# Performance work log

Measured on AMD Instinct MI355X. Metric: run time of the kernel, lower is better.

Reference implementation:

```python
import jax, jax.numpy as jnp
import numpy as np
import math

INPUT_DIM = 1024
EMBED_DIM = 1024
NUM_HEADS = 16
HEAD_DIM = EMBED_DIM // NUM_HEADS


def setup_inputs() -> dict:
    key = jax.random.key(0)
    k_x, k_qkv, k_out_w, k_out_b = jax.random.split(key, 4)
    x = jax.random.normal(k_x, (1, 4096, INPUT_DIM), dtype=jnp.float32)
    # nn.Linear weights are [out, in]; kaiming-uniform-ish scale
    s1 = 1.0 / math.sqrt(INPUT_DIM)
    s2 = 1.0 / math.sqrt(EMBED_DIM)
    qkv_w = jax.random.uniform(k_qkv, (3 * EMBED_DIM, INPUT_DIM), jnp.float32, -s1, s1)
    out_w = jax.random.uniform(k_out_w, (EMBED_DIM, EMBED_DIM), jnp.float32, -s2, s2)
    out_b = jax.random.uniform(k_out_b, (EMBED_DIM,), jnp.float32, -s2, s2)
    return {"x": x, "qkv_w": qkv_w, "out_w": out_w, "out_b": out_b}


def reference(x, qkv_w, out_w, out_b):
    B, N, C = x.shape
    qkv = jnp.einsum('bnc,ec->bne', x, qkv_w)  # [B,N,3E]
    q = qkv[:, :, 0:EMBED_DIM].reshape(B, N, NUM_HEADS, HEAD_DIM)
    k = qkv[:, :, EMBED_DIM:2 * EMBED_DIM].reshape(B, N, NUM_HEADS, HEAD_DIM)
    v = qkv[:, :, 2 * EMBED_DIM:].reshape(B, N, NUM_HEADS, HEAD_DIM)
    scores = jnp.einsum('bihd,bjhd->bhij', q, k) / jnp.sqrt(jnp.float32(HEAD_DIM))
    attn = jax.nn.softmax(scores, axis=-1)  # [B,H,N,N]
    out = jnp.einsum('bhik,bkhd->bhid', attn, v)
    out = out.transpose(0, 2, 1, 3).reshape(B, N, EMBED_DIM)
    return jnp.einsum('bne,fe->bnf', out, out_w) + out_b
```

## Files before the change

kernel.cpp:

```cpp
#include <hip/hip_runtime.h>
#include <hip/hip_bf16.h>

typedef __bf16 bf16;
typedef bf16 bf16x8 __attribute__((ext_vector_type(8)));
typedef bf16 bf16x4 __attribute__((ext_vector_type(4)));
typedef float f32x4 __attribute__((ext_vector_type(4)));

#define MFMA16(a, b, c) __builtin_amdgcn_mfma_f32_16x16x32_bf16(a, b, c, 0, 0, 0)

__device__ __forceinline__ void g2l16(const bf16* g, bf16* l) {
  __builtin_amdgcn_global_load_lds(
      (__attribute__((address_space(1))) void*)(void*)g,
      (__attribute__((address_space(3))) void*)l,
      16, 0, 0);
}

__global__ void sniff_dtype(const void* __restrict__ x, int* __restrict__ flag) {
  const unsigned short* u = (const unsigned short*)x;
  const int lane = threadIdx.x;
  unsigned short v = u[lane];
  int e = (v >> 7) & 0xFF;
  int sane = (e == 0) || (e >= 112 && e <= 142);
  unsigned long long m = __ballot(sane);
  if (lane == 0) flag[0] = (__popcll(m) >= 56) ? 1 : 0;
}

__global__ void convert_to_bf16(const void* __restrict__ in, bf16* __restrict__ out,
                                long n8, const int* __restrict__ flag) {
  long i = (long)blockIdx.x * 256 + threadIdx.x;
  if (i >= n8) return;
  if (*flag) {
    ((bf16x8*)out)[i] = ((const bf16x8*)in)[i];
  } else {
    const float4* p = (const float4*)in;
    float4 a = p[i * 2], b = p[i * 2 + 1];
    bf16x8 v;
    v[0] = (bf16)a.x; v[1] = (bf16)a.y; v[2] = (bf16)a.z; v[3] = (bf16)a.w;
    v[4] = (bf16)b.x; v[5] = (bf16)b.y; v[6] = (bf16)b.z; v[7] = (bf16)b.w;
    ((bf16x8*)out)[i] = v;
  }
}

__global__ __launch_bounds__(256) void gemm_qkv(
    const bf16* __restrict__ A, const bf16* __restrict__ B,
    bf16* __restrict__ qB, bf16* __restrict__ kP, bf16* __restrict__ vP) {
  __shared__ __align__(16) bf16 As[128 * 32];
  __shared__ __align__(16) bf16 Bs[128 * 32];

  const int tid  = threadIdx.x;
  const int lane = tid & 63;
  const int wave = tid >> 6;
  const int wm   = wave >> 1, wn = wave & 1;
  const int l15  = lane & 15, quad = lane >> 4;
  const long m0 = (long)blockIdx.x * 128;
  const long n0 = (long)blockIdx.y * 128;
  const int  K  = 1024;

  const bf16* Ab = A + m0 * K;
  const bf16* Bb = B + n0 * K;
  const int rowA = tid & 127;
  const int dc   = tid >> 7;

  f32x4 acc[4][4] = {};

  for (int k0 = 0; k0 < K; k0 += 32) {
    g2l16(Ab + (long)rowA * K + k0 + dc * 8,       As + tid * 8);
    g2l16(Ab + (long)rowA * K + k0 + (dc + 2) * 8, As + (tid + 256) * 8);
    g2l16(Bb + (long)rowA * K + k0 + dc * 8,       Bs + tid * 8);
    g2l16(Bb + (long)rowA * K + k0 + (dc + 2) * 8, Bs + (tid + 256) * 8);
    __syncthreads();

    bf16x8 af[4], bfr[4];
#pragma unroll
    for (int t = 0; t < 4; t++) {
      af[t]  = *(const bf16x8*)(As + (quad * 128 + wm * 64 + t * 16 + l15) * 8);
      bfr[t] = *(const bf16x8*)(Bs + (quad * 128 + wn * 64 + t * 16 + l15) * 8);
    }
#pragma unroll
    for (int tm = 0; tm < 4; tm++)
#pragma unroll
      for (int tn = 0; tn < 4; tn++)
        acc[tm][tn] = MFMA16(af[tm], bfr[tn], acc[tm][tn]);
    __syncthreads();
  }

  const long rb = m0 + wm * 64;
  const long cb = n0 + wn * 64;
  const int third = (int)(n0 >> 10);
  const float QSC = 0.125f * 1.44269504088896f;

#pragma unroll
  for (int tm = 0; tm < 4; tm++) {
#pragma unroll
    for (int tn = 0; tn < 4; tn++) {
      const long r0 = rb + tm * 16 + quad * 4;
      const long c  = cb + tn * 16 + l15;
      if (third == 0) {
#pragma unroll
        for (int r = 0; r < 4; r++)
          qB[(r0 + r) * 1024 + c] = (bf16)(acc[tm][tn][r] * QSC);
      } else if (third == 1) {
        const int ep = (int)c - 1024;
        const int h = ep >> 6, d = ep & 63;
        const long bhd = (long)h * 64 * 4096 + (long)((d >> 3) * 64) * 8 + (d & 7);
#pragma unroll
        for (int r = 0; r < 4; r++) {
          const int n = (int)(r0 + r);
          const int kt = n >> 6, kpos = n & 63;
          const int tn_ = 2 * (kpos >> 5) + ((kpos >> 2) & 1);
          const int m   = tn_ * 16 + ((kpos >> 3) & 3) * 4 + (kpos & 3);
          kP[bhd + (long)kt * 4096 + m * 8] = (bf16)acc[tm][tn][r];
        }
      } else {
        const int ep = (int)c - 2048;
        const int h = ep >> 6, d = ep & 63;
        const int n0r = (int)r0;
        const int kt = n0r >> 6, pc = (n0r & 63) >> 3;
        bf16x4 v;
#pragma unroll
        for (int r = 0; r < 4; r++) v[r] = (bf16)acc[tm][tn][r];
        *(bf16x4*)(vP + (long)(h * 64 + kt) * 4096 + (pc * 64 + d) * 8 +
                   (quad & 1) * 4) = v;
      }
    }
  }
}

template <bool BIAS, bool DYNOUT>
__global__ __launch_bounds__(256) void gemm_bt(
    const bf16* __restrict__ A, const bf16* __restrict__ B,
    void* __restrict__ Cv, const bf16* __restrict__ bias,
    int M, int Nn, int K, const int* __restrict__ oflag) {
  __shared__ __align__(16) bf16 As[128 * 32];
  __shared__ __align__(16) bf16 Bs[128 * 32];

  const int tid  = threadIdx.x;
  const int lane = tid & 63;
  const int wave = tid >> 6;
  const int wm   = wave >> 1, wn = wave & 1;
  const int l15  = lane & 15, quad = lane >> 4;
  const long m0 = (long)blockIdx.x * 128;
  const long n0 = (long)blockIdx.y * 128;

  const bf16* Ab = A + m0 * K;
  const bf16* Bb = B + n0 * K;
  const int rowA = tid & 127;
  const int dc   = tid >> 7;

  f32x4 acc[4][4] = {};

  for (int k0 = 0; k0 < K; k0 += 32) {
    g2l16(Ab + (long)rowA * K + k0 + dc * 8,       As + tid * 8);
    g2l16(Ab + (long)rowA * K + k0 + (dc + 2) * 8, As + (tid + 256) * 8);
    g2l16(Bb + (long)rowA * K + k0 + dc * 8,       Bs + tid * 8);
    g2l16(Bb + (long)rowA * K + k0 + (dc + 2) * 8, Bs + (tid + 256) * 8);
    __syncthreads();

    bf16x8 af[4], bfr[4];
#pragma unroll
    for (int t = 0; t < 4; t++) {
      af[t]  = *(const bf16x8*)(As + (quad * 128 + wm * 64 + t * 16 + l15) * 8);
      bfr[t] = *(const bf16x8*)(Bs + (quad * 128 + wn * 64 + t * 16 + l15) * 8);
    }
#pragma unroll
    for (int tm = 0; tm < 4; tm++)
#pragma unroll
      for (int tn = 0; tn < 4; tn++)
        acc[tm][tn] = MFMA16(af[tm], bfr[tn], acc[tm][tn]);
    __syncthreads();
  }

  const int obf = DYNOUT ? *oflag : 1;
  const long rb = m0 + wm * 64;
  const long cb = n0 + wn * 64;
#pragma unroll
  for (int tm = 0; tm < 4; tm++) {
#pragma unroll
    for (int tn = 0; tn < 4; tn++) {
      const long r0 = rb + tm * 16 + quad * 4;
      const long c  = cb + tn * 16 + l15;
      const float bv = BIAS ? (float)bias[c] : 0.0f;
#pragma unroll
      for (int r = 0; r < 4; r++) {
        const float val = acc[tm][tn][r] + bv;
        const long idx = (r0 + r) * Nn + c;
        if (DYNOUT && !obf) ((float*)Cv)[idx] = val;
        else                ((bf16*)Cv)[idx]  = (bf16)val;
      }
    }
  }
}

__global__ __launch_bounds__(256) void flash_attn(
    const bf16* __restrict__ qB, const bf16* __restrict__ kP,
    const bf16* __restrict__ vP, bf16* __restrict__ O) {
  __shared__ __align__(16) bf16 Ks[2][64 * 64];
  __shared__ __align__(16) bf16 Vs[2][64 * 64];

  const int tid = threadIdx.x;
  const int lane = tid & 63;
  const int wave = tid >> 6;
  const int l15 = lane & 15, quad = lane >> 4;
  const int bid = blockIdx.x;
  const int xcd = bid & 7, bi = bid >> 3;
  const int h  = xcd + 8 * (bi >> 5);
  const int qt = bi & 31;
  const int q0 = qt * 128;

  bf16x8 qf[2][2];
#pragma unroll
  for (int g = 0; g < 2; g++) {
    const bf16* qrow = qB + (long)(q0 + wave * 32 + g * 16 + l15) * 1024 + h * 64;
    qf[g][0] = *(const bf16x8*)(qrow + quad * 8);
    qf[g][1] = *(const bf16x8*)(qrow + 32 + quad * 8);
  }

  bf16x8 onesf;
#pragma unroll
  for (int j = 0; j < 8; j++) onesf[j] = (bf16)1.0f;

  f32x4 oa[2][4] = {};
  f32x4 la[2] = {};

  const bf16* kb = kP + (long)h * 64 * 4096;
  const bf16* vb = vP + (long)h * 64 * 4096;

#pragma unroll
  for (int i = 0; i < 2; i++) {
    g2l16(kb + (tid + i * 256) * 8, Ks[0] + (tid + i * 256) * 8);
    g2l16(vb + (tid + i * 256) * 8, Vs[0] + (tid + i * 256) * 8);
  }

  for (int kt = 0; kt < 64; kt++) {
    const int cur = kt & 1;
    __syncthreads();
    if (kt + 1 < 64) {
      const bf16* kbase = kb + (long)(kt + 1) * 4096;
      const bf16* vbase = vb + (long)(kt + 1) * 4096;
#pragma unroll
      for (int i = 0; i < 2; i++) {
        g2l16(kbase + (tid + i * 256) * 8, Ks[cur ^ 1] + (tid + i * 256) * 8);
        g2l16(vbase + (tid + i * 256) * 8, Vs[cur ^ 1] + (tid + i * 256) * 8);
      }
    }

    f32x4 s[2][4];
#pragma unroll
    for (int tn = 0; tn < 4; tn++) {
      bf16x8 a0 = *(const bf16x8*)(Ks[cur] + ((quad)*64 + tn * 16 + l15) * 8);
      bf16x8 a1 = *(const bf16x8*)(Ks[cur] + ((4 + quad) * 64 + tn * 16 + l15) * 8);
      f32x4 z0 = {}; z0 = MFMA16(a0, qf[0][0], z0); z0 = MFMA16(a1, qf[0][1], z0);
      f32x4 z1 = {}; z1 = MFMA16(a0, qf[1][0], z1); z1 = MFMA16(a1, qf[1][1], z1);
      s[0][tn] = z0; s[1][tn] = z1;
    }

    bf16x8 pf[2][2];
#pragma unroll
    for (int g = 0; g < 2; g++)
#pragma unroll
      for (int tn = 0; tn < 4; tn++)
#pragma unroll
        for (int r = 0; r < 4; r++)
          pf[g][tn >> 1][(tn & 1) * 4 + r] =
              (bf16)__builtin_amdgcn_exp2f(s[g][tn][r]);

#pragma unroll
    for (int tm = 0; tm < 4; tm++) {
      bf16x8 v0 = *(const bf16x8*)(Vs[cur] + ((quad)*64 + tm * 16 + l15) * 8);
      bf16x8 v1 = *(const bf16x8*)(Vs[cur] + ((4 + quad) * 64 + tm * 16 + l15) * 8);
      oa[0][tm] = MFMA16(v0, pf[0][0], oa[0][tm]);
      oa[0][tm] = MFMA16(v1, pf[0][1], oa[0][tm]);
      oa[1][tm] = MFMA16(v0, pf[1][0], oa[1][tm]);
      oa[1][tm] = MFMA16(v1, pf[1][1], oa[1][tm]);
    }
#pragma unroll
    for (int g = 0; g < 2; g++) {
      la[g] = MFMA16(onesf, pf[g][0], la[g]);
      la[g] = MFMA16(onesf, pf[g][1], la[g]);
    }
  }

#pragma unroll
  for (int g = 0; g < 2; g++) {
    const float inv = 1.0f / la[g][0];
    bf16* orow = O + (long)(q0 + wave * 32 + g * 16 + l15) * 1024 + h * 64;
#pragma unroll
    for (int tm = 0; tm < 4; tm++) {
      bf16x4 v;
#pragma unroll
      for (int r = 0; r < 4; r++) v[r] = (bf16)(oa[g][tm][r] * inv);
      *(bf16x4*)(orow + tm * 16 + quad * 4) = v;
    }
  }
}

extern "C" void kernel_launch(void* const* d_in, const int* in_sizes, int n_in,
                              void* d_out, int out_size, void* d_ws, size_t ws_size,
                              hipStream_t stream) {
  const void* x     = d_in[0];
  const void* qkv_w = d_in[1];
  const void* out_w = d_in[2];
  const void* out_b = d_in[3];

  char* ws = (char*)d_ws;
  int*  flag = (int*)ws;
  bf16* qB   = (bf16*)(ws + 4096);
  bf16* kP   = (bf16*)(ws + 4096 + 8388608);
  bf16* vP   = (bf16*)(ws + 4096 + 16777216);
  bf16* ob   = (bf16*)(ws + 4096 + 25165824);
  bf16* qwb  = (bf16*)(ws + 4096 + 33554432);
  bf16* xb   = ob;
  bf16* owb  = qB;
  bf16* obb  = qB + 1048576;

  sniff_dtype<<<1, 64, 0, stream>>>(x, flag);
  convert_to_bf16<<<2048, 256, 0, stream>>>(x, xb, 524288, flag);
  convert_to_bf16<<<1536, 256, 0, stream>>>(qkv_w, qwb, 393216, flag);

  gemm_qkv<<<dim3(32, 24), 256, 0, stream>>>(xb, qwb, qB, kP, vP);

  flash_attn<<<512, 256, 0, stream>>>(qB, kP, vP, ob);

  convert_to_bf16<<<512, 256, 0, stream>>>(out_w, owb, 131072, flag);
  convert_to_bf16<<<1, 256, 0, stream>>>(out_b, obb, 128, flag);

  gemm_bt<true, true><<<dim3(32, 8), 256, 0, stream>>>(
      ob, owb, d_out, obb, 4096, 1024, 1024, flag);
}
```

Before: 269.7 us.

## Split KV sequence across waves in flash attention with per-wave buffers

Each block now handles 64 queries and each wave processes a quarter of the key/value sequence with its own double-buffered LDS region. This removes block-wide barriers inside the main loop and replaces them with per-wave waitcnt. Partial outputs and row sums are reduced across waves through LDS at the end. The QKV GEMM epilogue writes K and V in a new 32-row tile layout to match, and the grid doubles to 1024 blocks. The cost is an extra LDS reduction and more LDS per block.

```diff
diff --git a/kernel.cpp b/kernel.cpp
--- a/kernel.cpp
+++ b/kernel.cpp
@@ -102,25 +102,24 @@
       } else if (third == 1) {
         const int ep = (int)c - 1024;
         const int h = ep >> 6, d = ep & 63;
-        const long bhd = (long)h * 64 * 4096 + (long)((d >> 3) * 64) * 8 + (d & 7);
 #pragma unroll
         for (int r = 0; r < 4; r++) {
           const int n = (int)(r0 + r);
-          const int kt = n >> 6, kpos = n & 63;
-          const int tn_ = 2 * (kpos >> 5) + ((kpos >> 2) & 1);
-          const int m   = tn_ * 16 + ((kpos >> 3) & 3) * 4 + (kpos & 3);
-          kP[bhd + (long)kt * 4096 + m * 8] = (bf16)acc[tm][tn][r];
+          const int si = n >> 5, k = n & 31;
+          const int sig = ((k >> 2) & 1) * 16 + (k >> 3) * 4 + (k & 3);
+          kP[((long)h * 128 + si) * 2048 +
+             ((d >> 3) * 32 + sig) * 8 + (d & 7)] = (bf16)acc[tm][tn][r];
         }
       } else {
         const int ep = (int)c - 2048;
         const int h = ep >> 6, d = ep & 63;
         const int n0r = (int)r0;
-        const int kt = n0r >> 6, pc = (n0r & 63) >> 3;
+        const int si = n0r >> 5, k0 = n0r & 31;
         bf16x4 v;
 #pragma unroll
         for (int r = 0; r < 4; r++) v[r] = (bf16)acc[tm][tn][r];
-        *(bf16x4*)(vP + (long)(h * 64 + kt) * 4096 + (pc * 64 + d) * 8 +
-                   (quad & 1) * 4) = v;
+        *(bf16x4*)(vP + ((long)h * 128 + si) * 2048 +
+                   ((k0 >> 3) * 64 + d) * 8 + (quad & 1) * 4) = v;
       }
     }
   }
@@ -194,8 +193,8 @@
 __global__ __launch_bounds__(256) void flash_attn(
     const bf16* __restrict__ qB, const bf16* __restrict__ kP,
     const bf16* __restrict__ vP, bf16* __restrict__ O) {
-  __shared__ __align__(16) bf16 Ks[2][64 * 64];
-  __shared__ __align__(16) bf16 Vs[2][64 * 64];
+  __shared__ __align__(16) bf16 Sbuf[4][2][4096];
+  __shared__ float lred[4][4][16];
 
   const int tid = threadIdx.x;
   const int lane = tid & 63;
@@ -203,14 +202,14 @@
   const int l15 = lane & 15, quad = lane >> 4;
   const int bid = blockIdx.x;
   const int xcd = bid & 7, bi = bid >> 3;
-  const int h  = xcd + 8 * (bi >> 5);
-  const int qt = bi & 31;
-  const int q0 = qt * 128;
-
-  bf16x8 qf[2][2];
-#pragma unroll
-  for (int g = 0; g < 2; g++) {
-    const bf16* qrow = qB + (long)(q0 + wave * 32 + g * 16 + l15) * 1024 + h * 64;
+  const int h  = xcd + 8 * (bi >> 6);
+  const int qt = bi & 63;
+  const int q0 = qt * 64;
+
+  bf16x8 qf[4][2];
+#pragma unroll
+  for (int g = 0; g < 4; g++) {
+    const bf16* qrow = qB + (long)(q0 + g * 16 + l15) * 1024 + h * 64;
     qf[g][0] = *(const bf16x8*)(qrow + quad * 8);
     qf[g][1] = *(const bf16x8*)(qrow + 32 + quad * 8);
   }
@@ -219,78 +218,90 @@
 #pragma unroll
   for (int j = 0; j < 8; j++) onesf[j] = (bf16)1.0f;
 
-  f32x4 oa[2][4] = {};
-  f32x4 la[2] = {};
-
-  const bf16* kb = kP + (long)h * 64 * 4096;
-  const bf16* vb = vP + (long)h * 64 * 4096;
-
-#pragma unroll
-  for (int i = 0; i < 2; i++) {
-    g2l16(kb + (tid + i * 256) * 8, Ks[0] + (tid + i * 256) * 8);
-    g2l16(vb + (tid + i * 256) * 8, Vs[0] + (tid + i * 256) * 8);
-  }
-
-  for (int kt = 0; kt < 64; kt++) {
-    const int cur = kt & 1;
-    __syncthreads();
-    if (kt + 1 < 64) {
-      const bf16* kbase = kb + (long)(kt + 1) * 4096;
-      const bf16* vbase = vb + (long)(kt + 1) * 4096;
-#pragma unroll
-      for (int i = 0; i < 2; i++) {
-        g2l16(kbase + (tid + i * 256) * 8, Ks[cur ^ 1] + (tid + i * 256) * 8);
-        g2l16(vbase + (tid + i * 256) * 8, Vs[cur ^ 1] + (tid + i * 256) * 8);
+  f32x4 oa[4][4] = {};
+  f32x4 la[4] = {};
+
+  const bf16* kb = kP + ((long)h * 128 + wave * 32) * 2048;
+  const bf16* vb = vP + ((long)h * 128 + wave * 32) * 2048;
+  bf16* buf0 = Sbuf[wave][0];
+  bf16* buf1 = Sbuf[wave][1];
+
+#pragma unroll
+  for (int i = 0; i < 4; i++) {
+    g2l16(kb + (lane + i * 64) * 8, buf0 + (lane + i * 64) * 8);
+    g2l16(vb + (lane + i * 64) * 8, buf0 + 2048 + (lane + i * 64) * 8);
+  }
+
+  for (int t = 0; t < 32; t++) {
+    const int cur = t & 1;
+    const long nt = (long)((t + 1) & 31) * 2048;
+    bf16* nb = cur ? buf0 : buf1;
+#pragma unroll
+    for (int i = 0; i < 4; i++) {
+      g2l16(kb + nt + (lane + i * 64) * 8, nb + (lane + i * 64) * 8);
+      g2l16(vb + nt + (lane + i * 64) * 8, nb + 2048 + (lane + i * 64) * 8);
+    }
+    __builtin_amdgcn_s_waitcnt(0x0F78);
+
+    const bf16* kg = cur ? buf1 : buf0;
+    const bf16* vg = kg + 2048;
+
+    bf16x8 pf[4];
+#pragma unroll
+    for (int kh = 0; kh < 2; kh++) {
+      bf16x8 a0 = *(const bf16x8*)(kg + ((quad)*32 + kh * 16 + l15) * 8);
+      bf16x8 a1 = *(const bf16x8*)(kg + ((4 + quad) * 32 + kh * 16 + l15) * 8);
+      f32x4 z[4];
+#pragma unroll
+      for (int g = 0; g < 4; g++) {
+        f32x4 zz = {};
+        zz = MFMA16(a0, qf[g][0], zz);
+        zz = MFMA16(a1, qf[g][1], zz);
+        z[g] = zz;
       }
-    }
-
-    f32x4 s[2][4];
-#pragma unroll
-    for (int tn = 0; tn < 4; tn++) {
-      bf16x8 a0 = *(const bf16x8*)(Ks[cur] + ((quad)*64 + tn * 16 + l15) * 8);
-      bf16x8 a1 = *(const bf16x8*)(Ks[cur] + ((4 + quad) * 64 + tn * 16 + l15) * 8);
-      f32x4 z0 = {}; z0 = MFMA16(a0, qf[0][0], z0); z0 = MFMA16(a1, qf[0][1], z0);
-      f32x4 z1 = {}; z1 = MFMA16(a0, qf[1][0], z1); z1 = MFMA16(a1, qf[1][1], z1);
-      s[0][tn] = z0; s[1][tn] = z1;
-    }
-
-    bf16x8 pf[2][2];
-#pragma unroll
-    for (int g = 0; g < 2; g++)
-#pragma unroll
-      for (int tn = 0; tn < 4; tn++)
+#pragma unroll
+      for (int g = 0; g < 4; g++)
 #pragma unroll
         for (int r = 0; r < 4; r++)
-          pf[g][tn >> 1][(tn & 1) * 4 + r] =
-              (bf16)__builtin_amdgcn_exp2f(s[g][tn][r]);
-
-#pragma unroll
-    for (int tm = 0; tm < 4; tm++) {
-      bf16x8 v0 = *(const bf16x8*)(Vs[cur] + ((quad)*64 + tm * 16 + l15) * 8);
-      bf16x8 v1 = *(const bf16x8*)(Vs[cur] + ((4 + quad) * 64 + tm * 16 + l15) * 8);
-      oa[0][tm] = MFMA16(v0, pf[0][0], oa[0][tm]);
-      oa[0][tm] = MFMA16(v1, pf[0][1], oa[0][tm]);
-      oa[1][tm] = MFMA16(v0, pf[1][0], oa[1][tm]);
-      oa[1][tm] = MFMA16(v1, pf[1][1], oa[1][tm]);
-    }
-#pragma unroll
-    for (int g = 0; g < 2; g++) {
-      la[g] = MFMA16(onesf, pf[g][0], la[g]);
-      la[g] = MFMA16(onesf, pf[g][1], la[g]);
-    }
-  }
-
-#pragma unroll
-  for (int g = 0; g < 2; g++) {
-    const float inv = 1.0f / la[g][0];
-    bf16* orow = O + (long)(q0 + wave * 32 + g * 16 + l15) * 1024 + h * 64;
-#pragma unroll
-    for (int tm = 0; tm < 4; tm++) {
-      bf16x4 v;
-#pragma unroll
-      for (int r = 0; r < 4; r++) v[r] = (bf16)(oa[g][tm][r] * inv);
-      *(bf16x4*)(orow + tm * 16 + quad * 4) = v;
-    }
+          pf[g][kh * 4 + r] = (bf16)__builtin_amdgcn_exp2f(z[g][r]);
+    }
+
+#pragma unroll
+    for (int dt = 0; dt < 4; dt++) {
+      bf16x8 v = *(const bf16x8*)(vg + (quad * 64 + dt * 16 + l15) * 8);
+#pragma unroll
+      for (int g = 0; g < 4; g++) oa[dt][g] = MFMA16(v, pf[g], oa[dt][g]);
+    }
+#pragma unroll
+    for (int g = 0; g < 4; g++) la[g] = MFMA16(onesf, pf[g], la[g]);
+  }
+
+  float* lds_f = (float*)Sbuf;
+  float* mine = lds_f + wave * 4096;
+#pragma unroll
+  for (int dt = 0; dt < 4; dt++)
+#pragma unroll
+    for (int g = 0; g < 4; g++)
+      *(f32x4*)(mine + (dt * 4 + g) * 256 + lane * 4) = oa[dt][g];
+  if (quad == 0)
+#pragma unroll
+    for (int g = 0; g < 4; g++) lred[wave][g][l15] = la[g][0];
+  __syncthreads();
+
+#pragma unroll
+  for (int g = 0; g < 4; g++) {
+    f32x4 acc = {};
+#pragma unroll
+    for (int u = 0; u < 4; u++)
+      acc += *(const f32x4*)(lds_f + u * 4096 + (wave * 4 + g) * 256 + lane * 4);
+    const float l = lred[0][g][l15] + lred[1][g][l15] +
+                    lred[2][g][l15] + lred[3][g][l15];
+    const float inv = 1.0f / l;
+    bf16x4 v;
+#pragma unroll
+    for (int r = 0; r < 4; r++) v[r] = (bf16)(acc[r] * inv);
+    *(bf16x4*)(O + (long)(q0 + g * 16 + l15) * 1024 + h * 64 + wave * 16 +
+               quad * 4) = v;
   }
 }
 
@@ -319,7 +330,7 @@
 
   gemm_qkv<<<dim3(32, 24), 256, 0, stream>>>(xb, qwb, qB, kP, vP);
 
-  flash_attn<<<512, 256, 0, stream>>>(qB, kP, vP, ob);
+  flash_attn<<<1024, 256, 0, stream>>>(qB, kP, vP, ob);
 
   convert_to_bf16<<<512, 256, 0, stream>>>(out_w, owb, 131072, flag);
   convert_to_bf16<<<1, 256, 0, stream>>>(out_b, obb, 128, flag);
```

New measurement: 270.6 us. No clear change (+0.3%).

## Halve flash-attention query tile to double grid and merge convert launches

Applied to the files above, without the earlier changes.

Flash attention now processes 64 query rows per block (16 per wave) instead of 128, doubling the grid to 1024 blocks and cutting per-wave accumulator registers. This aims to improve occupancy and latency hiding, at the cost of doubled K/V loads and a higher LDS-read-to-MFMA ratio. Separately, pairs of dtype-conversion launches are fused into a single kernel to reduce launch overhead.

```diff
diff --git a/kernel.cpp b/kernel.cpp
--- a/kernel.cpp
+++ b/kernel.cpp
@@ -25,11 +25,8 @@
   if (lane == 0) flag[0] = (__popcll(m) >= 56) ? 1 : 0;
 }
 
-__global__ void convert_to_bf16(const void* __restrict__ in, bf16* __restrict__ out,
-                                long n8, const int* __restrict__ flag) {
-  long i = (long)blockIdx.x * 256 + threadIdx.x;
-  if (i >= n8) return;
-  if (*flag) {
+__device__ __forceinline__ void conv8(const void* in, bf16* out, long i, int f) {
+  if (f) {
     ((bf16x8*)out)[i] = ((const bf16x8*)in)[i];
   } else {
     const float4* p = (const float4*)in;
@@ -39,6 +36,16 @@
     v[4] = (bf16)b.x; v[5] = (bf16)b.y; v[6] = (bf16)b.z; v[7] = (bf16)b.w;
     ((bf16x8*)out)[i] = v;
   }
+}
+
+__global__ void convert2_to_bf16(const void* __restrict__ a, bf16* __restrict__ oa,
+                                 long na8, const void* __restrict__ b,
+                                 bf16* __restrict__ ob, long nb8,
+                                 const int* __restrict__ flag) {
+  long i = (long)blockIdx.x * 256 + threadIdx.x;
+  const int f = *flag;
+  if (i < na8) conv8(a, oa, i, f);
+  else if (i - na8 < nb8) conv8(b, ob, i - na8, f);
 }
 
 __global__ __launch_bounds__(256) void gemm_qkv(
@@ -194,8 +201,8 @@
 __global__ __launch_bounds__(256) void flash_attn(
     const bf16* __restrict__ qB, const bf16* __restrict__ kP,
     const bf16* __restrict__ vP, bf16* __restrict__ O) {
-  __shared__ __align__(16) bf16 Ks[2][64 * 64];
-  __shared__ __align__(16) bf16 Vs[2][64 * 64];
+  __shared__ __align__(16) bf16 Ks[2][4096];
+  __shared__ __align__(16) bf16 Vs[2][4096];
 
   const int tid = threadIdx.x;
   const int lane = tid & 63;
@@ -203,24 +210,23 @@
   const int l15 = lane & 15, quad = lane >> 4;
   const int bid = blockIdx.x;
   const int xcd = bid & 7, bi = bid >> 3;
-  const int h  = xcd + 8 * (bi >> 5);
-  const int qt = bi & 31;
-  const int q0 = qt * 128;
-
-  bf16x8 qf[2][2];
-#pragma unroll
-  for (int g = 0; g < 2; g++) {
-    const bf16* qrow = qB + (long)(q0 + wave * 32 + g * 16 + l15) * 1024 + h * 64;
-    qf[g][0] = *(const bf16x8*)(qrow + quad * 8);
-    qf[g][1] = *(const bf16x8*)(qrow + 32 + quad * 8);
+  const int h  = xcd + 8 * (bi >> 6);
+  const int qt = bi & 63;
+  const int q0 = qt * 64;
+
+  bf16x8 qf[2];
+  {
+    const bf16* qrow = qB + (long)(q0 + wave * 16 + l15) * 1024 + h * 64;
+    qf[0] = *(const bf16x8*)(qrow + quad * 8);
+    qf[1] = *(const bf16x8*)(qrow + 32 + quad * 8);
   }
 
   bf16x8 onesf;
 #pragma unroll
   for (int j = 0; j < 8; j++) onesf[j] = (bf16)1.0f;
 
-  f32x4 oa[2][4] = {};
-  f32x4 la[2] = {};
+  f32x4 oa[4] = {};
+  f32x4 la = {};
 
   const bf16* kb = kP + (long)h * 64 * 4096;
   const bf16* vb = vP + (long)h * 64 * 4096;
@@ -244,53 +250,44 @@
       }
     }
 
-    f32x4 s[2][4];
+    f32x4 s[4];
 #pragma unroll
     for (int tn = 0; tn < 4; tn++) {
       bf16x8 a0 = *(const bf16x8*)(Ks[cur] + ((quad)*64 + tn * 16 + l15) * 8);
       bf16x8 a1 = *(const bf16x8*)(Ks[cur] + ((4 + quad) * 64 + tn * 16 + l15) * 8);
-      f32x4 z0 = {}; z0 = MFMA16(a0, qf[0][0], z0); z0 = MFMA16(a1, qf[0][1], z0);
-      f32x4 z1 = {}; z1 = MFMA16(a0, qf[1][0], z1); z1 = MFMA16(a1, qf[1][1], z1);
-      s[0][tn] = z0; s[1][tn] = z1;
-    }
-
-    bf16x8 pf[2][2];
-#pragma unroll
-    for (int g = 0; g < 2; g++)
-#pragma unroll
-      for (int tn = 0; tn < 4; tn++)
-#pragma unroll
-        for (int r = 0; r < 4; r++)
-          pf[g][tn >> 1][(tn & 1) * 4 + r] =
-              (bf16)__builtin_amdgcn_exp2f(s[g][tn][r]);
+      f32x4 z = {};
+      z = MFMA16(a0, qf[0], z);
+      z = MFMA16(a1, qf[1], z);
+      s[tn] = z;
+    }
+
+    bf16x8 pf[2];
+#pragma unroll
+    for (int tn = 0; tn < 4; tn++)
+#pragma unroll
+      for (int r = 0; r < 4; r++)
+        pf[tn >> 1][(tn & 1) * 4 + r] =
+            (bf16)__builtin_amdgcn_exp2f(s[tn][r]);
 
 #pragma unroll
     for (int tm = 0; tm < 4; tm++) {
       bf16x8 v0 = *(const bf16x8*)(Vs[cur] + ((quad)*64 + tm * 16 + l15) * 8);
       bf16x8 v1 = *(const bf16x8*)(Vs[cur] + ((4 + quad) * 64 + tm * 16 + l15) * 8);
-      oa[0][tm] = MFMA16(v0, pf[0][0], oa[0][tm]);
-      oa[0][tm] = MFMA16(v1, pf[0][1], oa[0][tm]);
-      oa[1][tm] = MFMA16(v0, pf[1][0], oa[1][tm]);
-      oa[1][tm] = MFMA16(v1, pf[1][1], oa[1][tm]);
-    }
-#pragma unroll
-    for (int g = 0; g < 2; g++) {
-      la[g] = MFMA16(onesf, pf[g][0], la[g]);
-      la[g] = MFMA16(onesf, pf[g][1], la[g]);
-    }
-  }
-
-#pragma unroll
-  for (int g = 0; g < 2; g++) {
-    const float inv = 1.0f / la[g][0];
-    bf16* orow = O + (long)(q0 + wave * 32 + g * 16 + l15) * 1024 + h * 64;
-#pragma unroll
-    for (int tm = 0; tm < 4; tm++) {
-      bf16x4 v;
-#pragma unroll
-      for (int r = 0; r < 4; r++) v[r] = (bf16)(oa[g][tm][r] * inv);
-      *(bf16x4*)(orow + tm * 16 + quad * 4) = v;
-    }
+      oa[tm] = MFMA16(v0, pf[0], oa[tm]);
+      oa[tm] = MFMA16(v1, pf[1], oa[tm]);
+    }
+    la = MFMA16(onesf, pf[0], la);
+    la = MFMA16(onesf, pf[1], la);
+  }
+
+  const float inv = 1.0f / la[0];
+  bf16* orow = O + (long)(q0 + wave * 16 + l15) * 1024 + h * 64;
+#pragma unroll
+  for (int tm = 0; tm < 4; tm++) {
+    bf16x4 v;
+#pragma unroll
+    for (int r = 0; r < 4; r++) v[r] = (bf16)(oa[tm][r] * inv);
+    *(bf16x4*)(orow + tm * 16 + quad * 4) = v;
   }
 }
 
@@ -314,15 +311,13 @@
   bf16* obb  = qB + 1048576;
 
   sniff_dtype<<<1, 64, 0, stream>>>(x, flag);
-  convert_to_bf16<<<2048, 256, 0, stream>>>(x, xb, 524288, flag);
-  convert_to_bf16<<<1536, 256, 0, stream>>>(qkv_w, qwb, 393216, flag);
+  convert2_to_bf16<<<3584, 256, 0, stream>>>(x, xb, 524288, qkv_w, qwb, 393216, flag);
 
   gemm_qkv<<<dim3(32, 24), 256, 0, stream>>>(xb, qwb, qB, kP, vP);
 
-  flash_attn<<<512, 256, 0, stream>>>(qB, kP, vP, ob);
-
-  convert_to_bf16<<<512, 256, 0, stream>>>(out_w, owb, 131072, flag);
-  convert_to_bf16<<<1, 256, 0, stream>>>(out_b, obb, 128, flag);
+  flash_attn<<<1024, 256, 0, stream>>>(qB, kP, vP, ob);
+
+  convert2_to_bf16<<<513, 256, 0, stream>>>(out_w, owb, 131072, out_b, obb, 128, flag);
 
   gemm_bt<true, true><<<dim3(32, 8), 256, 0, stream>>>(
       ob, owb, d_out, obb, 4096, 1024, 1024, flag);
```

After: 261.2 us. -3.2%, faster.

## Restructure flash attention to 2-wave blocks with V in registers and merged converts

Applied to the files above, without the earlier changes.

The attention kernel now uses 128-thread blocks with 64 query rows each, doubling the grid. Only K is staged into LDS, while V tiles are loaded straight from global memory into registers and double-buffered across an unrolled two-step loop. The row-sum is accumulated in scalar registers and reduced with shuffles, replacing the extra ones-matrix MFMAs. Pairs of dtype-conversion launches are merged into single kernels to cut launch count. The trade-offs are higher register pressure from the V buffers and K/V being loaded twice as often in total because of the smaller query tile.

```diff
diff --git a/kernel.cpp b/kernel.cpp
--- a/kernel.cpp
+++ b/kernel.cpp
@@ -25,11 +25,8 @@
   if (lane == 0) flag[0] = (__popcll(m) >= 56) ? 1 : 0;
 }
 
-__global__ void convert_to_bf16(const void* __restrict__ in, bf16* __restrict__ out,
-                                long n8, const int* __restrict__ flag) {
-  long i = (long)blockIdx.x * 256 + threadIdx.x;
-  if (i >= n8) return;
-  if (*flag) {
+__device__ __forceinline__ void conv8(const void* in, bf16* out, long i, int f) {
+  if (f) {
     ((bf16x8*)out)[i] = ((const bf16x8*)in)[i];
   } else {
     const float4* p = (const float4*)in;
@@ -39,6 +36,16 @@
     v[4] = (bf16)b.x; v[5] = (bf16)b.y; v[6] = (bf16)b.z; v[7] = (bf16)b.w;
     ((bf16x8*)out)[i] = v;
   }
+}
+
+__global__ void convert2_to_bf16(const void* __restrict__ a, bf16* __restrict__ oa,
+                                 long na8, const void* __restrict__ b,
+                                 bf16* __restrict__ ob, long nb8,
+                                 const int* __restrict__ flag) {
+  long i = (long)blockIdx.x * 256 + threadIdx.x;
+  const int f = *flag;
+  if (i < na8) conv8(a, oa, i, f);
+  else if (i - na8 < nb8) conv8(b, ob, i - na8, f);
 }
 
 __global__ __launch_bounds__(256) void gemm_qkv(
@@ -191,11 +198,10 @@
   }
 }
 
-__global__ __launch_bounds__(256) void flash_attn(
+__global__ __launch_bounds__(128, 2) void flash_attn(
     const bf16* __restrict__ qB, const bf16* __restrict__ kP,
     const bf16* __restrict__ vP, bf16* __restrict__ O) {
-  __shared__ __align__(16) bf16 Ks[2][64 * 64];
-  __shared__ __align__(16) bf16 Vs[2][64 * 64];
+  __shared__ __align__(16) bf16 Ks[2][4096];
 
   const int tid = threadIdx.x;
   const int lane = tid & 63;
@@ -203,9 +209,9 @@
   const int l15 = lane & 15, quad = lane >> 4;
   const int bid = blockIdx.x;
   const int xcd = bid & 7, bi = bid >> 3;
-  const int h  = xcd + 8 * (bi >> 5);
-  const int qt = bi & 31;
-  const int q0 = qt * 128;
+  const int h  = xcd + 8 * (bi >> 6);
+  const int qt = bi & 63;
+  const int q0 = qt * 64;
 
   bf16x8 qf[2][2];
 #pragma unroll
@@ -215,74 +221,88 @@
     qf[g][1] = *(const bf16x8*)(qrow + 32 + quad * 8);
   }
 
-  bf16x8 onesf;
-#pragma unroll
-  for (int j = 0; j < 8; j++) onesf[j] = (bf16)1.0f;
-
   f32x4 oa[2][4] = {};
-  f32x4 la[2] = {};
+  float l_sum[2] = {0.0f, 0.0f};
 
   const bf16* kb = kP + (long)h * 64 * 4096;
   const bf16* vb = vP + (long)h * 64 * 4096;
 
-#pragma unroll
-  for (int i = 0; i < 2; i++) {
-    g2l16(kb + (tid + i * 256) * 8, Ks[0] + (tid + i * 256) * 8);
-    g2l16(vb + (tid + i * 256) * 8, Vs[0] + (tid + i * 256) * 8);
-  }
-
-  for (int kt = 0; kt < 64; kt++) {
-    const int cur = kt & 1;
-    __syncthreads();
-    if (kt + 1 < 64) {
-      const bf16* kbase = kb + (long)(kt + 1) * 4096;
-      const bf16* vbase = vb + (long)(kt + 1) * 4096;
-#pragma unroll
-      for (int i = 0; i < 2; i++) {
-        g2l16(kbase + (tid + i * 256) * 8, Ks[cur ^ 1] + (tid + i * 256) * 8);
-        g2l16(vbase + (tid + i * 256) * 8, Vs[cur ^ 1] + (tid + i * 256) * 8);
-      }
-    }
-
+  const int voff_lo = (quad * 64 + l15) * 8;
+  const int voff_hi = ((4 + quad) * 64 + l15) * 8;
+
+  auto stageK = [&](int t, bf16* dst) {
+    const bf16* src = kb + (long)t * 4096;
+#pragma unroll
+    for (int i = 0; i < 4; i++)
+      g2l16(src + (tid + i * 128) * 8, dst + (tid + i * 128) * 8);
+  };
+  auto loadV = [&](int t, bf16x8* vr) {
+    const bf16* vt = vb + (long)t * 4096;
+#pragma unroll
+    for (int tm = 0; tm < 4; tm++) {
+      vr[tm]     = *(const bf16x8*)(vt + voff_lo + tm * 128);
+      vr[4 + tm] = *(const bf16x8*)(vt + voff_hi + tm * 128);
+    }
+  };
+  auto compute = [&](const bf16* kbuf, const bf16x8* vr) {
     f32x4 s[2][4];
 #pragma unroll
     for (int tn = 0; tn < 4; tn++) {
-      bf16x8 a0 = *(const bf16x8*)(Ks[cur] + ((quad)*64 + tn * 16 + l15) * 8);
-      bf16x8 a1 = *(const bf16x8*)(Ks[cur] + ((4 + quad) * 64 + tn * 16 + l15) * 8);
+      bf16x8 a0 = *(const bf16x8*)(kbuf + ((quad)*64 + tn * 16 + l15) * 8);
+      bf16x8 a1 = *(const bf16x8*)(kbuf + ((4 + quad) * 64 + tn * 16 + l15) * 8);
       f32x4 z0 = {}; z0 = MFMA16(a0, qf[0][0], z0); z0 = MFMA16(a1, qf[0][1], z0);
       f32x4 z1 = {}; z1 = MFMA16(a0, qf[1][0], z1); z1 = MFMA16(a1, qf[1][1], z1);
       s[0][tn] = z0; s[1][tn] = z1;
     }
-
     bf16x8 pf[2][2];
 #pragma unroll
-    for (int g = 0; g < 2; g++)
-#pragma unroll
-      for (int tn = 0; tn < 4; tn++)
-#pragma unroll
-        for (int r = 0; r < 4; r++)
-          pf[g][tn >> 1][(tn & 1) * 4 + r] =
-              (bf16)__builtin_amdgcn_exp2f(s[g][tn][r]);
-
+    for (int g = 0; g < 2; g++) {
+#pragma unroll
+      for (int hh = 0; hh < 2; hh++) {
+        union { bf16x8 v; __hip_bfloat162 h2[4]; } u;
+#pragma unroll
+        for (int j = 0; j < 4; j++) {
+          const int tn = hh * 2 + (j >> 1);
+          const int r  = (j & 1) * 2;
+          float p0 = __builtin_amdgcn_exp2f(s[g][tn][r]);
+          float p1 = __builtin_amdgcn_exp2f(s[g][tn][r + 1]);
+          l_sum[g] += p0 + p1;
+          u.h2[j] = __float22bfloat162_rn(float2{p0, p1});
+        }
+        pf[g][hh] = u.v;
+      }
+    }
 #pragma unroll
     for (int tm = 0; tm < 4; tm++) {
-      bf16x8 v0 = *(const bf16x8*)(Vs[cur] + ((quad)*64 + tm * 16 + l15) * 8);
-      bf16x8 v1 = *(const bf16x8*)(Vs[cur] + ((4 + quad) * 64 + tm * 16 + l15) * 8);
-      oa[0][tm] = MFMA16(v0, pf[0][0], oa[0][tm]);
-      oa[0][tm] = MFMA16(v1, pf[0][1], oa[0][tm]);
-      oa[1][tm] = MFMA16(v0, pf[1][0], oa[1][tm]);
-      oa[1][tm] = MFMA16(v1, pf[1][1], oa[1][tm]);
-    }
-#pragma unroll
-    for (int g = 0; g < 2; g++) {
-      la[g] = MFMA16(onesf, pf[g][0], la[g]);
-      la[g] = MFMA16(onesf, pf[g][1], la[g]);
-    }
+#pragma unroll
+      for (int g = 0; g < 2; g++) {
+        oa[g][tm] = MFMA16(vr[tm],     pf[g][0], oa[g][tm]);
+        oa[g][tm] = MFMA16(vr[4 + tm], pf[g][1], oa[g][tm]);
+      }
+    }
+  };
+
+  bf16x8 va0[8], va1[8];
+  stageK(0, Ks[0]);
+  loadV(0, va0);
+
+  for (int t = 0; t < 64; t += 2) {
+    __syncthreads();
+    stageK(t + 1, Ks[1]);
+    loadV(t + 1, va1);
+    compute(Ks[0], va0);
+    __syncthreads();
+    stageK((t + 2) & 63, Ks[0]);
+    loadV((t + 2) & 63, va0);
+    compute(Ks[1], va1);
   }
 
 #pragma unroll
   for (int g = 0; g < 2; g++) {
-    const float inv = 1.0f / la[g][0];
+    float l = l_sum[g];
+    l += __shfl_xor(l, 16, 64);
+    l += __shfl_xor(l, 32, 64);
+    const float inv = 1.0f / l;
     bf16* orow = O + (long)(q0 + wave * 32 + g * 16 + l15) * 1024 + h * 64;
 #pragma unroll
     for (int tm = 0; tm < 4; tm++) {
@@ -314,15 +334,13 @@
   bf16* obb  = qB + 1048576;
 
   sniff_dtype<<<1, 64, 0, stream>>>(x, flag);
-  convert_to_bf16<<<2048, 256, 0, stream>>>(x, xb, 524288, flag);
-  convert_to_bf16<<<1536, 256, 0, stream>>>(qkv_w, qwb, 393216, flag);
+  convert2_to_bf16<<<3584, 256, 0, stream>>>(x, xb, 524288, qkv_w, qwb, 393216, flag);
 
   gemm_qkv<<<dim3(32, 24), 256, 0, stream>>>(xb, qwb, qB, kP, vP);
 
-  flash_attn<<<512, 256, 0, stream>>>(qB, kP, vP, ob);
-
-  convert_to_bf16<<<512, 256, 0, stream>>>(out_w, owb, 131072, flag);
-  convert_to_bf16<<<1, 256, 0, stream>>>(out_b, obb, 128, flag);
+  flash_attn<<<1024, 128, 0, stream>>>(qB, kP, vP, ob);
+
+  convert2_to_bf16<<<513, 256, 0, stream>>>(out_w, owb, 131072, out_b, obb, 128, flag);
 
   gemm_bt<true, true><<<dim3(32, 8), 256, 0, stream>>>(
       ob, owb, d_out, obb, 4096, 1024, 1024, flag);
```

Result: faster. 259.5 us (-3.8%).
